# Kernel tuning notes

Hardware: AMD Instinct MI355X
Metric: run time of the kernel (lower is better)

## Reference

```python
import jax, jax.numpy as jnp
import numpy as np

HEADS = 32
KV_HEADS = 8
HEAD_DIM = 64
D = 2048
D_FF = 8192
EPS = 1e-6
THETA = 10000.0
MAX_STEPS = 4
NEG = -1e9


def _rope_tables(t):
    # LlamaRotaryEmbedding: cos/sin of shape [t, head_dim] with freqs duplicated
    inv_freq = 1.0 / (THETA ** (jnp.arange(0, HEAD_DIM, 2, dtype=jnp.float32) / HEAD_DIM))
    pos = jnp.arange(t, dtype=jnp.float32)
    freqs = pos[:, None] * inv_freq[None, :]          # [t, hd/2]
    emb = jnp.concatenate([freqs, freqs], axis=-1)    # [t, hd]
    return jnp.cos(emb), jnp.sin(emb)


def _rotate_half(x):
    h = x.shape[-1] // 2
    return jnp.concatenate([-x[..., h:], x[..., :h]], axis=-1)


def _rms_norm(x, w):
    return x * jax.lax.rsqrt(jnp.mean(x * x, axis=-1, keepdims=True) + EPS) * w


def _decoder_layer(h, w_q, w_k, w_v, w_o, ln1_w, ln2_w, w_gate, w_up, w_down):
    # h: [N, t, D]
    N, t, _ = h.shape
    x = _rms_norm(h, ln1_w)
    q = (x @ w_q).reshape(N, t, HEADS, HEAD_DIM)
    k = (x @ w_k).reshape(N, t, KV_HEADS, HEAD_DIM)
    v = (x @ w_v).reshape(N, t, KV_HEADS, HEAD_DIM)
    cos, sin = _rope_tables(t)
    cos = cos[None, :, None, :]
    sin = sin[None, :, None, :]
    q = q * cos + _rotate_half(q) * sin
    k = k * cos + _rotate_half(k) * sin
    rep = HEADS // KV_HEADS
    k = jnp.repeat(k, rep, axis=2)  # GQA: repeat kv heads
    v = jnp.repeat(v, rep, axis=2)
    scores = jnp.einsum('bqhd,bkhd->bhqk', q, k) / jnp.sqrt(jnp.float32(HEAD_DIM))
    causal = jnp.tril(jnp.ones((t, t), dtype=bool))
    scores = jnp.where(causal[None, None], scores, NEG)
    attn = jax.nn.softmax(scores, axis=-1)
    o = jnp.einsum('bhqk,bkhd->bqhd', attn, v).reshape(N, t, HEADS * HEAD_DIM)
    h = h + o @ w_o
    x = _rms_norm(h, ln2_w)
    h = h + (jax.nn.silu(x @ w_gate) * (x @ w_up)) @ w_down
    return h


def _micro_step_decode(hiddens, w_q, w_k, w_v, w_o, ln1_w, ln2_w, w_gate, w_up, w_down):
    # hiddens: [N, 1, D]; loop recomputes full attention over growing sequence (no KV cache)
    out = None
    for _ in range(MAX_STEPS + 1):
        out = _decoder_layer(hiddens, w_q, w_k, w_v, w_o, ln1_w, ln2_w, w_gate, w_up, w_down)
        hiddens = jnp.concatenate([hiddens, out[:, -1:, :]], axis=1)
    return out  # [N, MAX_STEPS+1, D]


def _gather_indices(comp_seq_lens, inst_lens):
    seqs = np.asarray(comp_seq_lens)
    insts = np.asarray(inst_lens)
    idx, off = [], 0
    for s, i in zip(seqs, insts):
        s, i = int(s), int(i)
        idx.append(np.arange(off + i - 1, off + s - 1))  # take_off_last=True
        off += s
    return np.concatenate(idx)


def setup_inputs() -> dict:
    key = jax.random.key(0)
    ks = jax.random.split(key, 10)
    B, S, I = 8, 512, 256
    total = B * S
    w = 0.02
    return {
        'hidden_states': jax.random.normal(ks[0], (1, total, D), jnp.float32),
        'comp_seq_lens': jnp.full((B,), S, dtype=jnp.int64),
        'inst_lens': jnp.full((B,), I, dtype=jnp.int64),
        'w_q': jax.random.normal(ks[1], (D, HEADS * HEAD_DIM), jnp.float32) * w,
        'w_k': jax.random.normal(ks[2], (D, KV_HEADS * HEAD_DIM), jnp.float32) * w,
        'w_v': jax.random.normal(ks[3], (D, KV_HEADS * HEAD_DIM), jnp.float32) * w,
        'w_o': jax.random.normal(ks[4], (HEADS * HEAD_DIM, D), jnp.float32) * w,
        'ln1_w': jnp.ones((D,), jnp.float32),
        'ln2_w': jnp.ones((D,), jnp.float32),
        'w_gate': jax.random.normal(ks[5], (D, D_FF), jnp.float32) * w,
        'w_up': jax.random.normal(ks[6], (D, D_FF), jnp.float32) * w,
        'w_down': jax.random.normal(ks[7], (D_FF, D), jnp.float32) * w,
    }


def reference(hidden_states, comp_seq_lens, inst_lens, w_q, w_k, w_v, w_o, ln1_w, ln2_w, w_gate, w_up, w_down):
    idx = _gather_indices(comp_seq_lens, inst_lens)
    hiddens = hidden_states[0, idx][:, None, :]  # [N, 1, D]
    return _micro_step_decode(hiddens, w_q, w_k, w_v, w_o, ln1_w, ln2_w, w_gate, w_up, w_down)
```

## Files before the change

kernel.cpp:

```cpp
#include <hip/hip_runtime.h>
#include <hip/hip_bf16.h>
#include <stdint.h>

#define DMODEL 2048
#define QDIM   2048
#define KVDIM  512
#define QKVDIM 3072
#define DFF    8192
#define NSTEPS 5

typedef __bf16 bf16_t;
typedef __attribute__((ext_vector_type(8))) __bf16 bf16x8;
typedef __attribute__((ext_vector_type(4))) float f32x4;

#define GLL16(g, l)                                                         \
  __builtin_amdgcn_global_load_lds(                                          \
      (const __attribute__((address_space(1))) void*)(g),                    \
      (__attribute__((address_space(3))) void*)(l), 16, 0, 0)

#define MFMA_BF16 __builtin_amdgcn_mfma_f32_16x16x32_bf16

__device__ __forceinline__ float wave_sum(float v) {
#pragma unroll
  for (int o = 32; o > 0; o >>= 1) v += __shfl_xor(v, o, 64);
  return v;
}

__global__ void build_idx_kernel(const int* __restrict__ seq, const int* __restrict__ inst,
                                 int B, int* __restrict__ idx, int* __restrict__ dN, int nmax) {
  __shared__ int sbase[64], soff[64], scnt[64], snb;
  if (threadIdx.x == 0) {
    bool is64 = (B >= 2);
    for (int i = 0; i < B && is64; ++i) {
      if (i & 1) { if (seq[i] != 0 || inst[i] != 0) is64 = false; }
      else       { if (seq[i] == 0) is64 = false; }
    }
    int off = 0, row = 0, nb = (B < 64 ? B : 64);
    for (int b = 0; b < nb; ++b) {
      int s = is64 ? seq[2 * b] : seq[b];
      int i = is64 ? inst[2 * b] : inst[b];
      sbase[b] = row; soff[b] = off + i - 1; scnt[b] = s - i;
      row += s - i; off += s;
    }
    snb = nb;
    *dN = row < nmax ? row : nmax;
  }
  __syncthreads();
  int nb = snb;
  for (int b = 0; b < nb; ++b) {
    int cnt = scnt[b], base = sbase[b], o0 = soff[b];
    for (int t = threadIdx.x; t < cnt; t += blockDim.x) {
      int r = base + t;
      if (r < nmax) idx[r] = o0 + t;
    }
  }
}

__global__ __launch_bounds__(256)
void gather_kernel(const float* __restrict__ hs, const int* __restrict__ idx,
                   float* __restrict__ h0, const int* __restrict__ dN) {
  int r = blockIdx.x; if (r >= *dN) return;
  const float4* in = (const float4*)(hs + (size_t)idx[r] * DMODEL);
  float4* out = (float4*)(h0 + (size_t)r * DMODEL);
  out[threadIdx.x]       = in[threadIdx.x];
  out[threadIdx.x + 256] = in[threadIdx.x + 256];
}

__global__ __launch_bounds__(256)
void wtrans_kernel(const float* __restrict__ W, bf16_t* __restrict__ Wt, int K, int Nc) {
  __shared__ float tile[32][33];
  int c0 = blockIdx.x * 32, k0 = blockIdx.y * 32;
  int tx = threadIdx.x & 31, ty = threadIdx.x >> 5;
#pragma unroll
  for (int yy = 0; yy < 4; ++yy)
    tile[ty + 8 * yy][tx] = W[(size_t)(k0 + ty + 8 * yy) * Nc + c0 + tx];
  __syncthreads();
#pragma unroll
  for (int yy = 0; yy < 4; ++yy)
    Wt[(size_t)(c0 + ty + 8 * yy) * K + k0 + tx] = (bf16_t)tile[tx][ty + 8 * yy];
}

__global__ __launch_bounds__(256)
void rmsnorm_kernel(const float* __restrict__ h, long hstride, const float* __restrict__ w,
                    bf16_t* __restrict__ x, const int* __restrict__ dN) {
  int r = blockIdx.x; if (r >= *dN) return;
  const float* row = h + (size_t)r * hstride;
  int t = threadIdx.x;
  float4 v0 = ((const float4*)row)[2 * t];
  float4 v1 = ((const float4*)row)[2 * t + 1];
  float ss = v0.x*v0.x + v0.y*v0.y + v0.z*v0.z + v0.w*v0.w
           + v1.x*v1.x + v1.y*v1.y + v1.z*v1.z + v1.w*v1.w;
  ss = wave_sum(ss);
  __shared__ float part[4];
  if ((t & 63) == 0) part[t >> 6] = ss;
  __syncthreads();
  float inv = rsqrtf((part[0] + part[1] + part[2] + part[3]) * (1.0f / DMODEL) + 1e-6f);
  const float4* wv = (const float4*)w;
  float4 w0 = wv[2 * t], w1 = wv[2 * t + 1];
  union { bf16_t b[8]; uint4 q; } u;
  u.b[0] = (bf16_t)(v0.x * inv * w0.x);
  u.b[1] = (bf16_t)(v0.y * inv * w0.y);
  u.b[2] = (bf16_t)(v0.z * inv * w0.z);
  u.b[3] = (bf16_t)(v0.w * inv * w0.w);
  u.b[4] = (bf16_t)(v1.x * inv * w1.x);
  u.b[5] = (bf16_t)(v1.y * inv * w1.y);
  u.b[6] = (bf16_t)(v1.z * inv * w1.z);
  u.b[7] = (bf16_t)(v1.w * inv * w1.w);
  *(uint4*)(x + (size_t)r * DMODEL + t * 8) = u.q;
}

__global__ __launch_bounds__(512)
void rope_cache_kernel(const bf16_t* __restrict__ qkv, bf16_t* __restrict__ kc,
                       bf16_t* __restrict__ vc, int p, const int* __restrict__ dN) {
  int r = blockIdx.x; if (r >= *dN) return;
  int d = threadIdx.x;
  int e = d & 63, fi = e & 31;
  size_t qb = (size_t)r * QKVDIM;
  float k  = (float)qkv[qb + QDIM + d];
  float kp = (float)qkv[qb + QDIM + (d ^ 32)];
  float ang = (float)p * expf((float)fi * -0.28782313662425576f);
  float cv, sv; sincosf(ang, &sv, &cv);
  float kr = k * cv + ((e < 32) ? -kp : kp) * sv;
  size_t cb = ((size_t)r * NSTEPS + p) * KVDIM + d;
  kc[cb] = (bf16_t)kr;
  vc[cb] = qkv[qb + QDIM + KVDIM + d];
}

__global__ __launch_bounds__(256)
void attn_kernel(const bf16_t* __restrict__ qkv, const bf16_t* __restrict__ kc,
                 const bf16_t* __restrict__ vc, bf16_t* __restrict__ o,
                 int p, const int* __restrict__ dN) {
  int r = blockIdx.x; if (r >= *dN) return;
  int wid = threadIdx.x >> 6, lane = threadIdx.x & 63;
  int head = blockIdx.y * 4 + wid;
  int kh = head >> 2;
  float q = (float)qkv[(size_t)r * QKVDIM + head * 64 + lane];
  int fi = lane & 31;
  float ang = (float)p * expf((float)fi * -0.28782313662425576f);
  float cv, sv; sincosf(ang, &sv, &cv);
  float qp = __shfl_xor(q, 32, 64);
  float qr = q * cv + ((lane < 32) ? -qp : qp) * sv;
  size_t cbase = (size_t)r * NSTEPS * KVDIM + kh * 64 + lane;
  float s[NSTEPS];
#pragma unroll
  for (int j = 0; j < NSTEPS; ++j) {
    s[j] = -1e30f;
    if (j <= p) {
      float kj = (float)kc[cbase + (size_t)j * KVDIM];
      s[j] = wave_sum(qr * kj) * 0.125f;
    }
  }
  float m = s[0];
#pragma unroll
  for (int j = 1; j < NSTEPS; ++j) m = fmaxf(m, s[j]);
  float aw[NSTEPS]; float den = 0.f;
#pragma unroll
  for (int j = 0; j < NSTEPS; ++j) { aw[j] = (j <= p) ? expf(s[j] - m) : 0.f; den += aw[j]; }
  float oa = 0.f;
#pragma unroll
  for (int j = 0; j < NSTEPS; ++j)
    if (j <= p) oa += aw[j] * (float)vc[cbase + (size_t)j * KVDIM];
  o[(size_t)r * QDIM + head * 64 + lane] = (bf16_t)(oa / den);
}

template <int MODE>
__global__ __launch_bounds__(256)
void gemm_kernel(const bf16_t* __restrict__ A, const bf16_t* __restrict__ Bt, int K,
                 const int* __restrict__ dN,
                 float* __restrict__ outf, long ostride,
                 const float* __restrict__ res, long rstride,
                 bf16_t* __restrict__ outb, long obstride) {
  const int N = *dN;
  const int brow = blockIdx.y * 128, bcol = blockIdx.x * 128;
  if (brow >= N) return;

  __shared__ __align__(16) bf16_t As[2][128 * 32];
  __shared__ __align__(16) bf16_t Bs[2][128 * 32];
  const int t = threadIdx.x;
  const int lane = t & 63, wid = t >> 6;
  const int wr = wid >> 1, wc = wid & 1;
  const int hi = lane >> 4, lo = lane & 15;
  const int xk = (lo >> 1) & 3;

  const int srow = wid * 16 + (lane >> 2);
  const int kseg = ((lane & 3) ^ ((lane >> 3) & 3)) * 8;
  const bf16_t* gA0 = A  + (size_t)(brow + srow) * K + kseg;
  const bf16_t* gA1 = gA0 + (size_t)64 * K;
  const bf16_t* gB0 = Bt + (size_t)(bcol + srow) * K + kseg;
  const bf16_t* gB1 = gB0 + (size_t)64 * K;
  const int lofs = wid * 512;

  f32x4 acc[4][4] = {};
  const int nk = K >> 5;

  GLL16(gA0, &As[0][lofs]);
  GLL16(gA1, &As[0][2048 + lofs]);
  GLL16(gB0, &Bs[0][lofs]);
  GLL16(gB1, &Bs[0][2048 + lofs]);

  int cur = 0;
  for (int kt = 0; kt < nk; ++kt) {
    __syncthreads();
    if (kt + 1 < nk) {
      const int k1 = (kt + 1) << 5;
      GLL16(gA0 + k1, &As[cur ^ 1][lofs]);
      GLL16(gA1 + k1, &As[cur ^ 1][2048 + lofs]);
      GLL16(gB0 + k1, &Bs[cur ^ 1][lofs]);
      GLL16(gB1 + k1, &Bs[cur ^ 1][2048 + lofs]);
    }
    bf16x8 af[4], bfr[4];
#pragma unroll
    for (int m = 0; m < 4; ++m)
      af[m] = *(const bf16x8*)(&As[cur][(wr * 64 + m * 16 + lo) * 32 + (hi ^ xk) * 8]);
#pragma unroll
    for (int n = 0; n < 4; ++n)
      bfr[n] = *(const bf16x8*)(&Bs[cur][(wc * 64 + n * 16 + lo) * 32 + (hi ^ xk) * 8]);
#pragma unroll
    for (int m = 0; m < 4; ++m)
#pragma unroll
      for (int n = 0; n < 4; ++n)
        acc[m][n] = MFMA_BF16(af[m], bfr[n], acc[m][n], 0, 0, 0);
    cur ^= 1;
  }

  const int rbase = brow + wr * 64 + hi * 4;
  const int cbase = bcol + wc * 64 + lo;
#pragma unroll
  for (int m = 0; m < 4; ++m) {
#pragma unroll
    for (int n = 0; n < 4; ++n) {
      const int col = cbase + n * 16;
#pragma unroll
      for (int j = 0; j < 4; ++j) {
        const int row = rbase + m * 16 + j;
        if (row < N) {
          float v = acc[m][n][j];
          if (MODE == 0) {
            outb[(size_t)row * obstride + col] = (bf16_t)v;
          } else {
            outf[(size_t)row * ostride + col] = res[(size_t)row * rstride + col] + v;
          }
        }
      }
    }
  }
}

template <int MODE>
__global__ __launch_bounds__(512)
void gemm256_kernel(const bf16_t* __restrict__ A, const bf16_t* __restrict__ Bt,
                    int krow, int kchunk, const int* __restrict__ dN,
                    long zstride,
                    bf16_t* __restrict__ outb, long obstride,
                    const bf16_t* __restrict__ gateb, long gstride) {
  const int N = *dN;
  const int brow = blockIdx.y * 256, bcol = blockIdx.x * 256;
  if (brow >= N) return;
  const size_t koff = (size_t)blockIdx.z * kchunk;

  extern __shared__ __align__(16) bf16_t lds[];
  bf16_t* As = lds;
  bf16_t* Bs = lds + 32768;

  const int t = threadIdx.x;
  const int lane = t & 63, wid = t >> 6;
  const int wm = wid >> 2, wn = wid & 3;
  const int hi = lane >> 4, lo = lane & 15;

  const int swsrc = ((lane & 3) ^ ((lane >> 3) & 3)) << 3;
  const size_t aoffl = (size_t)(brow + (lane >> 2)) * krow + koff + swsrc;
  const size_t boffl = (size_t)(bcol + (lane >> 2)) * krow + koff + swsrc;
  const size_t chk0 = (size_t)(wid * 32) * krow;
  const size_t chk1 = (size_t)(wid * 32 + 16) * krow;
  const int lst0 = wid * 1024;
  const int lst1 = wid * 1024 + 512;

  const int rsl = (hi ^ ((lo >> 1) & 3)) * 8;
  const int abase = (wm * 128 + lo) * 32 + rsl;
  const int bbase = (wn * 64 + lo) * 32 + rsl;

  f32x4 acc[8][4] = {};
  const int nt = kchunk >> 6;

#define STG_A(T, kh) do {                                        \
    const bf16_t* g_ = A + aoffl + (size_t)(T) * 64 + (kh) * 32; \
    bf16_t* l_ = As + (((T) & 1) << 14) + (kh) * 8192;           \
    GLL16(g_ + chk0, l_ + lst0);                                 \
    GLL16(g_ + chk1, l_ + lst1);                                 \
  } while (0)
#define STG_B(T, kh) do {                                        \
    const bf16_t* g_ = Bt + boffl + (size_t)(T) * 64 + (kh) * 32;\
    bf16_t* l_ = Bs + (((T) & 1) << 14) + (kh) * 8192;           \
    GLL16(g_ + chk0, l_ + lst0);                                 \
    GLL16(g_ + chk1, l_ + lst1);                                 \
  } while (0)

  STG_A(0, 0); STG_B(0, 0); STG_A(0, 1); STG_B(0, 1);
  if (nt > 1) {
    STG_A(1, 0); STG_B(1, 0);
    asm volatile("s_waitcnt vmcnt(8)" ::: "memory");
  } else {
    asm volatile("s_waitcnt vmcnt(4)" ::: "memory");
  }
  __builtin_amdgcn_s_barrier();

  for (int T = 0; T < nt; ++T) {
    const int buf = (T & 1) << 14;
    bf16x8 af[8], b0, b1;
#pragma unroll
    for (int m = 0; m < 8; ++m)
      af[m] = *(const bf16x8*)(As + buf + abase + m * 512);
    b0 = *(const bf16x8*)(Bs + buf + bbase);
    b1 = *(const bf16x8*)(Bs + buf + bbase + 512);
    if (T + 1 < nt) STG_A(T + 1, 1);
    asm volatile("s_waitcnt lgkmcnt(0)" ::: "memory");
    __builtin_amdgcn_s_barrier();
    __builtin_amdgcn_s_setprio(1);
#pragma unroll
    for (int m = 0; m < 8; ++m) {
      acc[m][0] = MFMA_BF16(af[m], b0, acc[m][0], 0, 0, 0);
      acc[m][1] = MFMA_BF16(af[m], b1, acc[m][1], 0, 0, 0);
    }
    __builtin_amdgcn_s_setprio(0);
    b0 = *(const bf16x8*)(Bs + buf + bbase + 1024);
    b1 = *(const bf16x8*)(Bs + buf + bbase + 1536);
    if (T + 1 < nt) STG_B(T + 1, 1);
    if (T < nt - 1) asm volatile("s_waitcnt vmcnt(8) lgkmcnt(0)" ::: "memory");
    else            asm volatile("s_waitcnt vmcnt(0) lgkmcnt(0)" ::: "memory");
    __builtin_amdgcn_s_barrier();
    __builtin_amdgcn_s_setprio(1);
#pragma unroll
    for (int m = 0; m < 8; ++m) {
      acc[m][2] = MFMA_BF16(af[m], b0, acc[m][2], 0, 0, 0);
      acc[m][3] = MFMA_BF16(af[m], b1, acc[m][3], 0, 0, 0);
    }
    __builtin_amdgcn_s_setprio(0);
#pragma unroll
    for (int m = 0; m < 8; ++m)
      af[m] = *(const bf16x8*)(As + buf + 8192 + abase + m * 512);
    b0 = *(const bf16x8*)(Bs + buf + 8192 + bbase);
    b1 = *(const bf16x8*)(Bs + buf + 8192 + bbase + 512);
    if (T + 2 < nt) STG_A(T + 2, 0);
    asm volatile("s_waitcnt lgkmcnt(0)" ::: "memory");
    __builtin_amdgcn_s_barrier();
    __builtin_amdgcn_s_setprio(1);
#pragma unroll
    for (int m = 0; m < 8; ++m) {
      acc[m][0] = MFMA_BF16(af[m], b0, acc[m][0], 0, 0, 0);
      acc[m][1] = MFMA_BF16(af[m], b1, acc[m][1], 0, 0, 0);
    }
    __builtin_amdgcn_s_setprio(0);
    b0 = *(const bf16x8*)(Bs + buf + 8192 + bbase + 1024);
    b1 = *(const bf16x8*)(Bs + buf + 8192 + bbase + 1536);
    if (T + 2 < nt) STG_B(T + 2, 0);
    if (T < nt - 2)       asm volatile("s_waitcnt vmcnt(8) lgkmcnt(0)" ::: "memory");
    else if (T == nt - 2) asm volatile("s_waitcnt vmcnt(4) lgkmcnt(0)" ::: "memory");
    else                  asm volatile("s_waitcnt vmcnt(0) lgkmcnt(0)" ::: "memory");
    __builtin_amdgcn_s_barrier();
    __builtin_amdgcn_s_setprio(1);
#pragma unroll
    for (int m = 0; m < 8; ++m) {
      acc[m][2] = MFMA_BF16(af[m], b0, acc[m][2], 0, 0, 0);
      acc[m][3] = MFMA_BF16(af[m], b1, acc[m][3], 0, 0, 0);
    }
    __builtin_amdgcn_s_setprio(0);
  }
#undef STG_A
#undef STG_B

  const int rbase = brow + wm * 128 + hi * 4;
  const int cbase = bcol + wn * 64 + lo;
  bf16_t* pb = (MODE == 3) ? outb + (size_t)blockIdx.z * zstride : outb;
#pragma unroll
  for (int m = 0; m < 8; ++m) {
#pragma unroll
    for (int n = 0; n < 4; ++n) {
      const int col = cbase + n * 16;
#pragma unroll
      for (int j = 0; j < 4; ++j) {
        const int row = rbase + m * 16 + j;
        if (row < N) {
          float v = acc[m][n][j];
          if (MODE == 2) {
            float g = (float)gateb[(size_t)row * gstride + col];
            float sg = g / (1.0f + expf(-g));
            pb[(size_t)row * obstride + col] = (bf16_t)(sg * v);
          } else {
            pb[(size_t)row * obstride + col] = (bf16_t)v;
          }
        }
      }
    }
  }
}

__global__ __launch_bounds__(256)
void reduce_down_kernel(const bf16_t* __restrict__ part, long zstride,
                        const float* __restrict__ res, float* __restrict__ out,
                        const int* __restrict__ dN) {
  int r = blockIdx.x; if (r >= *dN) return;
  const int c = threadIdx.x * 8;
  float s[8] = {};
#pragma unroll
  for (int z = 0; z < 4; ++z) {
    const bf16x8 v = *(const bf16x8*)(part + (size_t)z * zstride + (size_t)r * DMODEL + c);
#pragma unroll
    for (int j = 0; j < 8; ++j) s[j] += (float)v[j];
  }
  const float* rv = res + (size_t)r * DMODEL + c;
  float* o = out + (size_t)r * (NSTEPS * DMODEL) + c;
#pragma unroll
  for (int j = 0; j < 8; ++j) o[j] = s[j] + rv[j];
}

extern "C" void kernel_launch(void* const* d_in, const int* in_sizes, int n_in,
                              void* d_out, int out_size, void* d_ws, size_t ws_size,
                              hipStream_t stream) {
  const float* hs  = (const float*)d_in[0];
  const int*   seq = (const int*)d_in[1];
  const int*   ins = (const int*)d_in[2];
  const float* w_q = (const float*)d_in[3];
  const float* w_k = (const float*)d_in[4];
  const float* w_v = (const float*)d_in[5];
  const float* w_o = (const float*)d_in[6];
  const float* ln1 = (const float*)d_in[7];
  const float* ln2 = (const float*)d_in[8];
  const float* w_g = (const float*)d_in[9];
  const float* w_u = (const float*)d_in[10];
  const float* w_d = (const float*)d_in[11];
  const int  B     = in_sizes[1];
  const long total = (long)in_sizes[0] / DMODEL;

  const size_t WQKV_E = (size_t)QKVDIM * DMODEL;
  const size_t WO_E   = (size_t)DMODEL * DMODEL;
  const size_t WG_E   = (size_t)DFF * DMODEL;

  struct WS {
    int* dN; int* idx;
    bf16_t *Wqkv, *Wo, *Wg, *Wu, *Wd;
    bf16_t* kc; bf16_t* vc; float* hattn; bf16_t* gate;
    float* h0; bf16_t* x; bf16_t* qkv; bf16_t* o;
    bf16_t* part;
    size_t bytes;
  };
  char* base = (char*)d_ws;
  auto mk = [&](long nm) {
    WS w; size_t o = 0;
    auto alloc = [&](size_t b) { char* p = base + o; o = (o + b + 255) & ~(size_t)255; return p; };
    w.dN    = (int*)alloc(4);
    w.idx   = (int*)alloc((size_t)nm * 4);
    w.Wqkv  = (bf16_t*)alloc(WQKV_E * 2);
    w.Wo    = (bf16_t*)alloc(WO_E * 2);
    w.Wg    = (bf16_t*)alloc(WG_E * 2);
    w.Wu    = (bf16_t*)alloc(WG_E * 2);
    w.Wd    = (bf16_t*)alloc(WG_E * 2);
    w.kc    = (bf16_t*)alloc((size_t)nm * NSTEPS * KVDIM * 2);
    w.vc    = (bf16_t*)alloc((size_t)nm * NSTEPS * KVDIM * 2);
    w.hattn = (float*)alloc((size_t)nm * DMODEL * 4);
    w.gate  = (bf16_t*)alloc((size_t)nm * DFF * 2);
    w.h0    = (float*)alloc((size_t)nm * DMODEL * 4);
    w.x     = (bf16_t*)alloc((size_t)nm * DMODEL * 2);
    w.qkv   = (bf16_t*)alloc((size_t)nm * QKVDIM * 2);
    w.o     = (bf16_t*)alloc((size_t)nm * DMODEL * 2);
    w.part  = (bf16_t*)w.h0;
    w.bytes = o;
    return w;
  };
  long nm = ((total + 255) / 256) * 256;
  WS w = mk(nm);
  while (w.bytes > ws_size && nm > 256) { nm -= 256; w = mk(nm); }

  build_idx_kernel<<<1, 512, 0, stream>>>(seq, ins, B, w.idx, w.dN, (int)nm);
  gather_kernel<<<(uint32_t)nm, 256, 0, stream>>>(hs, w.idx, w.h0, w.dN);

  dim3 tb(256);
  wtrans_kernel<<<dim3(DMODEL/32, DMODEL/32), tb, 0, stream>>>(w_q, w.Wqkv, DMODEL, DMODEL);
  wtrans_kernel<<<dim3(KVDIM/32,  DMODEL/32), tb, 0, stream>>>(w_k, w.Wqkv + (size_t)QDIM * DMODEL, DMODEL, KVDIM);
  wtrans_kernel<<<dim3(KVDIM/32,  DMODEL/32), tb, 0, stream>>>(w_v, w.Wqkv + (size_t)(QDIM + KVDIM) * DMODEL, DMODEL, KVDIM);
  wtrans_kernel<<<dim3(DMODEL/32, DMODEL/32), tb, 0, stream>>>(w_o, w.Wo, DMODEL, DMODEL);
  wtrans_kernel<<<dim3(DFF/32,    DMODEL/32), tb, 0, stream>>>(w_g, w.Wg, DMODEL, DFF);
  wtrans_kernel<<<dim3(DFF/32,    DMODEL/32), tb, 0, stream>>>(w_u, w.Wu, DMODEL, DFF);
  wtrans_kernel<<<dim3(DMODEL/32, DFF/32),    tb, 0, stream>>>(w_d, w.Wd, DFF, DMODEL);

  const int gy  = (int)(nm / 128);
  const int gy2 = (int)(nm / 256);
  const uint32_t LDSB = 131072;
  float* outF = (float*)d_out;
  const long zs = (long)nm * DMODEL;

  for (int p = 0; p < NSTEPS; ++p) {
    const float* hprev = (p == 0) ? w.h0 : outF + (size_t)(p - 1) * DMODEL;
    const long   hstr  = (p == 0) ? DMODEL : (long)NSTEPS * DMODEL;

    rmsnorm_kernel<<<(uint32_t)nm, 256, 0, stream>>>(hprev, hstr, ln1, w.x, w.dN);

    gemm_kernel<0><<<dim3(QKVDIM/128, gy), 256, 0, stream>>>(w.x, w.Wqkv, DMODEL, w.dN,
        nullptr, 0, nullptr, 0, w.qkv, QKVDIM);

    rope_cache_kernel<<<(uint32_t)nm, 512, 0, stream>>>(w.qkv, w.kc, w.vc, p, w.dN);
    attn_kernel<<<dim3((uint32_t)nm, 8), 256, 0, stream>>>(w.qkv, w.kc, w.vc, w.o, p, w.dN);

    gemm_kernel<1><<<dim3(DMODEL/128, gy), 256, 0, stream>>>(w.o, w.Wo, DMODEL, w.dN,
        w.hattn, DMODEL, hprev, hstr, nullptr, 0);

    rmsnorm_kernel<<<(uint32_t)nm, 256, 0, stream>>>(w.hattn, DMODEL, ln2, w.x, w.dN);

    gemm256_kernel<0><<<dim3(DFF/256, gy2, 1), 512, LDSB, stream>>>(w.x, w.Wg, DMODEL, DMODEL,
        w.dN, 0, w.gate, DFF, nullptr, 0);

    gemm256_kernel<2><<<dim3(DFF/256, gy2, 1), 512, LDSB, stream>>>(w.x, w.Wu, DMODEL, DMODEL,
        w.dN, 0, w.gate, DFF, w.gate, DFF);

    gemm256_kernel<3><<<dim3(DMODEL/256, gy2, 4), 512, LDSB, stream>>>(w.gate, w.Wd, DFF, DFF/4,
        w.dN, zs, w.part, DMODEL, nullptr, 0);
    reduce_down_kernel<<<(uint32_t)nm, 256, 0, stream>>>(
        w.part, zs, w.hattn, outF + (size_t)p * DMODEL, w.dN);
  }
}
```

Measured before the change: 2.079 ms.

## Use split-K 256-tile GEMM for QKV/O projections and fuse reductions with RMSNorm

Replaces the 128-tile GEMM for the QKV and output projections with the 256-tile split-K GEMM, adding partial-sum reduce kernels. The residual add and the next RMSNorm are fused into those reduce kernels, which removes the separate rmsnorm launches after step 0. Workspace is reordered so partial buffers alias the gate and qkv storage. The cost is extra partial-sum traffic, an extra bf16 rounding of the partials, and fewer blocks per launch at small N.

```diff
diff --git a/kernel.cpp b/kernel.cpp
--- a/kernel.cpp
+++ b/kernel.cpp
@@ -164,89 +164,6 @@
 }
 
 template <int MODE>
-__global__ __launch_bounds__(256)
-void gemm_kernel(const bf16_t* __restrict__ A, const bf16_t* __restrict__ Bt, int K,
-                 const int* __restrict__ dN,
-                 float* __restrict__ outf, long ostride,
-                 const float* __restrict__ res, long rstride,
-                 bf16_t* __restrict__ outb, long obstride) {
-  const int N = *dN;
-  const int brow = blockIdx.y * 128, bcol = blockIdx.x * 128;
-  if (brow >= N) return;
-
-  __shared__ __align__(16) bf16_t As[2][128 * 32];
-  __shared__ __align__(16) bf16_t Bs[2][128 * 32];
-  const int t = threadIdx.x;
-  const int lane = t & 63, wid = t >> 6;
-  const int wr = wid >> 1, wc = wid & 1;
-  const int hi = lane >> 4, lo = lane & 15;
-  const int xk = (lo >> 1) & 3;
-
-  const int srow = wid * 16 + (lane >> 2);
-  const int kseg = ((lane & 3) ^ ((lane >> 3) & 3)) * 8;
-  const bf16_t* gA0 = A  + (size_t)(brow + srow) * K + kseg;
-  const bf16_t* gA1 = gA0 + (size_t)64 * K;
-  const bf16_t* gB0 = Bt + (size_t)(bcol + srow) * K + kseg;
-  const bf16_t* gB1 = gB0 + (size_t)64 * K;
-  const int lofs = wid * 512;
-
-  f32x4 acc[4][4] = {};
-  const int nk = K >> 5;
-
-  GLL16(gA0, &As[0][lofs]);
-  GLL16(gA1, &As[0][2048 + lofs]);
-  GLL16(gB0, &Bs[0][lofs]);
-  GLL16(gB1, &Bs[0][2048 + lofs]);
-
-  int cur = 0;
-  for (int kt = 0; kt < nk; ++kt) {
-    __syncthreads();
-    if (kt + 1 < nk) {
-      const int k1 = (kt + 1) << 5;
-      GLL16(gA0 + k1, &As[cur ^ 1][lofs]);
-      GLL16(gA1 + k1, &As[cur ^ 1][2048 + lofs]);
-      GLL16(gB0 + k1, &Bs[cur ^ 1][lofs]);
-      GLL16(gB1 + k1, &Bs[cur ^ 1][2048 + lofs]);
-    }
-    bf16x8 af[4], bfr[4];
-#pragma unroll
-    for (int m = 0; m < 4; ++m)
-      af[m] = *(const bf16x8*)(&As[cur][(wr * 64 + m * 16 + lo) * 32 + (hi ^ xk) * 8]);
-#pragma unroll
-    for (int n = 0; n < 4; ++n)
-      bfr[n] = *(const bf16x8*)(&Bs[cur][(wc * 64 + n * 16 + lo) * 32 + (hi ^ xk) * 8]);
-#pragma unroll
-    for (int m = 0; m < 4; ++m)
-#pragma unroll
-      for (int n = 0; n < 4; ++n)
-        acc[m][n] = MFMA_BF16(af[m], bfr[n], acc[m][n], 0, 0, 0);
-    cur ^= 1;
-  }
-
-  const int rbase = brow + wr * 64 + hi * 4;
-  const int cbase = bcol + wc * 64 + lo;
-#pragma unroll
-  for (int m = 0; m < 4; ++m) {
-#pragma unroll
-    for (int n = 0; n < 4; ++n) {
-      const int col = cbase + n * 16;
-#pragma unroll
-      for (int j = 0; j < 4; ++j) {
-        const int row = rbase + m * 16 + j;
-        if (row < N) {
-          float v = acc[m][n][j];
-          if (MODE == 0) {
-            outb[(size_t)row * obstride + col] = (bf16_t)v;
-          } else {
-            outf[(size_t)row * ostride + col] = res[(size_t)row * rstride + col] + v;
-          }
-        }
-      }
-    }
-  }
-}
-
-template <int MODE>
 __global__ __launch_bounds__(512)
 void gemm256_kernel(const bf16_t* __restrict__ A, const bf16_t* __restrict__ Bt,
                     int krow, int kchunk, const int* __restrict__ dN,
@@ -394,23 +311,55 @@
   }
 }
 
+__global__ __launch_bounds__(384)
+void reduce_qkv_kernel(const bf16_t* __restrict__ part, long zstride,
+                       bf16_t* __restrict__ out, const int* __restrict__ dN) {
+  int r = blockIdx.x; if (r >= *dN) return;
+  const int c = threadIdx.x * 8;
+  const bf16x8 a = *(const bf16x8*)(part + (size_t)r * QKVDIM + c);
+  const bf16x8 b = *(const bf16x8*)(part + zstride + (size_t)r * QKVDIM + c);
+  union { bf16_t v[8]; uint4 q; } u;
+#pragma unroll
+  for (int j = 0; j < 8; ++j) u.v[j] = (bf16_t)((float)a[j] + (float)b[j]);
+  *(uint4*)(out + (size_t)r * QKVDIM + c) = u.q;
+}
+
+template <int NZ>
 __global__ __launch_bounds__(256)
-void reduce_down_kernel(const bf16_t* __restrict__ part, long zstride,
-                        const float* __restrict__ res, float* __restrict__ out,
+void reduce_norm_kernel(const bf16_t* __restrict__ part, long zstride,
+                        const float* __restrict__ res, long rstride,
+                        float* __restrict__ out, long ostride,
+                        bf16_t* __restrict__ x, const float* __restrict__ lnw,
                         const int* __restrict__ dN) {
   int r = blockIdx.x; if (r >= *dN) return;
   const int c = threadIdx.x * 8;
-  float s[8] = {};
-#pragma unroll
-  for (int z = 0; z < 4; ++z) {
+  const float* rv = res + (size_t)r * rstride + c;
+  float s[8];
+#pragma unroll
+  for (int j = 0; j < 8; ++j) s[j] = rv[j];
+#pragma unroll
+  for (int z = 0; z < NZ; ++z) {
     const bf16x8 v = *(const bf16x8*)(part + (size_t)z * zstride + (size_t)r * DMODEL + c);
 #pragma unroll
     for (int j = 0; j < 8; ++j) s[j] += (float)v[j];
   }
-  const float* rv = res + (size_t)r * DMODEL + c;
-  float* o = out + (size_t)r * (NSTEPS * DMODEL) + c;
-#pragma unroll
-  for (int j = 0; j < 8; ++j) o[j] = s[j] + rv[j];
+  float* o = out + (size_t)r * ostride + c;
+#pragma unroll
+  for (int j = 0; j < 8; ++j) o[j] = s[j];
+  if (x) {
+    float ss = 0.f;
+#pragma unroll
+    for (int j = 0; j < 8; ++j) ss += s[j] * s[j];
+    ss = wave_sum(ss);
+    __shared__ float ps[4];
+    if ((threadIdx.x & 63) == 0) ps[threadIdx.x >> 6] = ss;
+    __syncthreads();
+    float inv = rsqrtf((ps[0] + ps[1] + ps[2] + ps[3]) * (1.0f / DMODEL) + 1e-6f);
+    union { bf16_t b[8]; uint4 q; } u;
+#pragma unroll
+    for (int j = 0; j < 8; ++j) u.b[j] = (bf16_t)(s[j] * inv * lnw[c + j]);
+    *(uint4*)(x + (size_t)r * DMODEL + c) = u.q;
+  }
 }
 
 extern "C" void kernel_launch(void* const* d_in, const int* in_sizes, int n_in,
@@ -439,7 +388,7 @@
     int* dN; int* idx;
     bf16_t *Wqkv, *Wo, *Wg, *Wu, *Wd;
     bf16_t* kc; bf16_t* vc; float* hattn; bf16_t* gate;
-    float* h0; bf16_t* x; bf16_t* qkv; bf16_t* o;
+    bf16_t* qkv; bf16_t* o; float* h0; bf16_t* x;
     bf16_t* part;
     size_t bytes;
   };
@@ -458,11 +407,11 @@
     w.vc    = (bf16_t*)alloc((size_t)nm * NSTEPS * KVDIM * 2);
     w.hattn = (float*)alloc((size_t)nm * DMODEL * 4);
     w.gate  = (bf16_t*)alloc((size_t)nm * DFF * 2);
+    w.qkv   = (bf16_t*)alloc((size_t)nm * QKVDIM * 2);
+    w.o     = (bf16_t*)alloc((size_t)nm * DMODEL * 2);
     w.h0    = (float*)alloc((size_t)nm * DMODEL * 4);
     w.x     = (bf16_t*)alloc((size_t)nm * DMODEL * 2);
-    w.qkv   = (bf16_t*)alloc((size_t)nm * QKVDIM * 2);
-    w.o     = (bf16_t*)alloc((size_t)nm * DMODEL * 2);
-    w.part  = (bf16_t*)w.h0;
+    w.part  = (bf16_t*)w.qkv;
     w.bytes = o;
     return w;
   };
@@ -482,38 +431,40 @@
   wtrans_kernel<<<dim3(DFF/32,    DMODEL/32), tb, 0, stream>>>(w_u, w.Wu, DMODEL, DFF);
   wtrans_kernel<<<dim3(DMODEL/32, DFF/32),    tb, 0, stream>>>(w_d, w.Wd, DFF, DMODEL);
 
-  const int gy  = (int)(nm / 128);
   const int gy2 = (int)(nm / 256);
   const uint32_t LDSB = 131072;
   float* outF = (float*)d_out;
-  const long zs = (long)nm * DMODEL;
+  const long zsD = (long)nm * DMODEL;
+  const long zsQ = (long)nm * QKVDIM;
 
   for (int p = 0; p < NSTEPS; ++p) {
     const float* hprev = (p == 0) ? w.h0 : outF + (size_t)(p - 1) * DMODEL;
     const long   hstr  = (p == 0) ? DMODEL : (long)NSTEPS * DMODEL;
 
-    rmsnorm_kernel<<<(uint32_t)nm, 256, 0, stream>>>(hprev, hstr, ln1, w.x, w.dN);
-
-    gemm_kernel<0><<<dim3(QKVDIM/128, gy), 256, 0, stream>>>(w.x, w.Wqkv, DMODEL, w.dN,
-        nullptr, 0, nullptr, 0, w.qkv, QKVDIM);
+    if (p == 0)
+      rmsnorm_kernel<<<(uint32_t)nm, 256, 0, stream>>>(hprev, hstr, ln1, w.x, w.dN);
+
+    gemm256_kernel<3><<<dim3(QKVDIM/256, gy2, 2), 512, LDSB, stream>>>(
+        w.x, w.Wqkv, DMODEL, DMODEL/2, w.dN, zsQ, w.gate, QKVDIM, nullptr, 0);
+    reduce_qkv_kernel<<<(uint32_t)nm, 384, 0, stream>>>(w.gate, zsQ, w.qkv, w.dN);
 
     rope_cache_kernel<<<(uint32_t)nm, 512, 0, stream>>>(w.qkv, w.kc, w.vc, p, w.dN);
     attn_kernel<<<dim3((uint32_t)nm, 8), 256, 0, stream>>>(w.qkv, w.kc, w.vc, w.o, p, w.dN);
 
-    gemm_kernel<1><<<dim3(DMODEL/128, gy), 256, 0, stream>>>(w.o, w.Wo, DMODEL, w.dN,
-        w.hattn, DMODEL, hprev, hstr, nullptr, 0);
-
-    rmsnorm_kernel<<<(uint32_t)nm, 256, 0, stream>>>(w.hattn, DMODEL, ln2, w.x, w.dN);
-
-    gemm256_kernel<0><<<dim3(DFF/256, gy2, 1), 512, LDSB, stream>>>(w.x, w.Wg, DMODEL, DMODEL,
-        w.dN, 0, w.gate, DFF, nullptr, 0);
-
-    gemm256_kernel<2><<<dim3(DFF/256, gy2, 1), 512, LDSB, stream>>>(w.x, w.Wu, DMODEL, DMODEL,
-        w.dN, 0, w.gate, DFF, w.gate, DFF);
-
-    gemm256_kernel<3><<<dim3(DMODEL/256, gy2, 4), 512, LDSB, stream>>>(w.gate, w.Wd, DFF, DFF/4,
-        w.dN, zs, w.part, DMODEL, nullptr, 0);
-    reduce_down_kernel<<<(uint32_t)nm, 256, 0, stream>>>(
-        w.part, zs, w.hattn, outF + (size_t)p * DMODEL, w.dN);
-  }
-}
+    gemm256_kernel<3><<<dim3(DMODEL/256, gy2, 4), 512, LDSB, stream>>>(
+        w.o, w.Wo, DMODEL, DMODEL/4, w.dN, zsD, w.gate, DMODEL, nullptr, 0);
+    reduce_norm_kernel<4><<<(uint32_t)nm, 256, 0, stream>>>(
+        w.gate, zsD, hprev, hstr, w.hattn, DMODEL, w.x, ln2, w.dN);
+
+    gemm256_kernel<0><<<dim3(DFF/256, gy2, 1), 512, LDSB, stream>>>(
+        w.x, w.Wg, DMODEL, DMODEL, w.dN, 0, w.gate, DFF, nullptr, 0);
+    gemm256_kernel<2><<<dim3(DFF/256, gy2, 1), 512, LDSB, stream>>>(
+        w.x, w.Wu, DMODEL, DMODEL, w.dN, 0, w.gate, DFF, w.gate, DFF);
+
+    gemm256_kernel<3><<<dim3(DMODEL/256, gy2, 4), 512, LDSB, stream>>>(
+        w.gate, w.Wd, DFF, DFF/4, w.dN, zsD, w.part, DMODEL, nullptr, 0);
+    reduce_norm_kernel<4><<<(uint32_t)nm, 256, 0, stream>>>(
+        w.part, zsD, w.hattn, DMODEL, outF + (size_t)p * DMODEL, (long)NSTEPS * DMODEL,
+        (p + 1 < NSTEPS) ? w.x : nullptr, ln1, w.dN);
+  }
+}
```

New measurement: 1.897 ms. 8.8% less time.
